# Optimization experiments

Hardware: AMD Instinct MI355X
Metric: run time of the kernel (lower is better)

## Reference

```python
import jax, jax.numpy as jnp
import numpy as np

D, B, L, LS, DH, DU, QK, CD = 5, 2048, 50, 50, 128, 128, 64, 64
EPS = 1e-5

def _l2norm(x):
    n = jnp.linalg.norm(x, axis=-1, keepdims=True)
    return x / jnp.maximum(n, 1e-12)

def setup_inputs() -> dict:
    key = jax.random.key(0)
    ks = jax.random.split(key, 20)
    def pw(k, shape):
        return jax.random.normal(k, shape, dtype=jnp.float32) * 0.02
    return {
        "u": jax.random.normal(ks[0], (B, DU), jnp.float32),
        "H_intra": jax.random.normal(ks[1], (D, B, L, DH), jnp.float32),
        "H_share": jax.random.normal(ks[2], (B, LS, DH), jnp.float32),
        "h": jax.random.normal(ks[3], (B, DH), jnp.float32),
        "domain_ids": jax.random.randint(ks[4], (B,), 0, D),
        "Wq": pw(ks[5], (DU + DH, QK)), "bq": jnp.zeros((QK,), jnp.float32),
        "Wki": pw(ks[6], (DH, QK)), "bki": jnp.zeros((QK,), jnp.float32),
        "Wvi": pw(ks[7], (DH, QK)), "bvi": jnp.zeros((QK,), jnp.float32),
        "Wks": pw(ks[8], (DH, QK)), "bks": jnp.zeros((QK,), jnp.float32),
        "Wvs": pw(ks[9], (DH, QK)), "bvs": jnp.zeros((QK,), jnp.float32),
        "Wf": pw(ks[10], (2 * QK, CD)), "bf": jnp.zeros((CD,), jnp.float32),
        "Wgb": pw(ks[11], (CD, 2 * DH)), "bgb": jnp.zeros((2 * DH,), jnp.float32),
    }

def reference(u, H_intra, H_share, h, domain_ids, Wq, bq, Wki, bki, Wvi, bvi,
              Wks, bks, Wvs, bvs, Wf, bf, Wgb, bgb):
    scale = jnp.sqrt(jnp.asarray(QK, jnp.float32))
    # ---- CDIExtractor (domain loop batched over leading D axis) ----
    c = H_intra.mean(axis=2)                                   # [D,B,DH] ctx = mean over L
    u_b = jnp.broadcast_to(u, (D, B, DU))
    Q = jnp.concatenate([u_b, c], axis=-1) @ Wq + bq            # [D,B,QK]
    Ki = H_intra @ Wki + bki                                    # [D,B,L,QK]
    Vi = H_intra @ Wvi + bvi
    Ks = H_share @ Wks + bks                                    # [B,LS,QK]
    Vs = H_share @ Wvs + bvs
    a_i = jax.nn.softmax(jnp.einsum('dbq,dblq->dbl', Q, Ki) / scale, axis=-1)
    h_i = jnp.einsum('dbl,dblq->dbq', a_i, Vi)                  # [D,B,QK]
    a_s = jax.nn.softmax(jnp.einsum('dbq,blq->dbl', Q, Ks) / scale, axis=-1)
    h_s = jnp.einsum('dbl,blq->dbq', a_s, Vs)                   # [D,B,QK]
    z = jnp.concatenate([h_i, h_s], axis=-1) @ Wf + bf          # [D,B,CD]
    # ---- contrastive loss (stacked as [B,D,QK] like torch.stack(dim=1)) ----
    hi = jnp.transpose(h_i, (1, 0, 2))
    hs = jnp.transpose(h_s, (1, 0, 2))
    ni, ns = _l2norm(hi), _l2norm(hs)
    pos_sim = jnp.sum(ni * ns, axis=-1)                         # [B,D]
    all_sim = jnp.einsum('bdq,beq->bde', ni, ni)                # [B,D,D]
    denom = jnp.exp(all_sim).sum(axis=-1)                       # [B,D]
    L_con = -jnp.mean(jnp.log(jnp.exp(pos_sim) / (denom + 1e-8) + 1e-8))
    # ---- CDIRInjector_Norm (domain-masked AdaNorm, segment statistics) ----
    onehot = jax.nn.one_hot(domain_ids, D, dtype=h.dtype)       # [B,D]
    cnt = jnp.maximum(onehot.sum(axis=0), 1.0)                  # [D]
    mean_d = (onehot.T @ h) / cnt[:, None]                      # [D,DH]
    var_d = (onehot.T @ (h * h)) / cnt[:, None] - mean_d ** 2   # biased var
    mu = mean_d[domain_ids]                                     # [B,DH]
    va = var_d[domain_ids]
    h_norm = (h - mu) / jnp.sqrt(va + EPS)
    z_sel = z[domain_ids, jnp.arange(B)]                        # [B,CD]
    gb = z_sel @ Wgb + bgb
    gamma, beta = jnp.split(gb, 2, axis=-1)
    out = gamma * h_norm + beta + h                             # [B,DH]
    return out, L_con
```

## Files before the change

### kernel.cpp

```cpp
#include <hip/hip_runtime.h>
#include <math.h>

#define D 5
#define B 2048
#define L 50
#define LS 50
#define DH 128
#define DU 128
#define QK 64
#define CD 64
#define EPS 1e-5f

__device__ __forceinline__ float wsum(float v) {
    v += __shfl_xor(v, 1, 64);
    v += __shfl_xor(v, 2, 64);
    v += __shfl_xor(v, 4, 64);
    v += __shfl_xor(v, 8, 64);
    v += __shfl_xor(v, 16, 64);
    v += __shfl_xor(v, 32, 64);
    return v;
}

__device__ __forceinline__ float wmax(float v) {
    v = fmaxf(v, __shfl_xor(v, 1, 64));
    v = fmaxf(v, __shfl_xor(v, 2, 64));
    v = fmaxf(v, __shfl_xor(v, 4, 64));
    v = fmaxf(v, __shfl_xor(v, 8, 64));
    v = fmaxf(v, __shfl_xor(v, 16, 64));
    v = fmaxf(v, __shfl_xor(v, 32, 64));
    return v;
}

__device__ __forceinline__ float gsum32(float v) {
    v += __shfl_xor(v, 1, 64);
    v += __shfl_xor(v, 2, 64);
    v += __shfl_xor(v, 4, 64);
    v += __shfl_xor(v, 8, 64);
    v += __shfl_xor(v, 16, 64);
    return v;
}

__device__ __forceinline__ float dot4(float4 a, float4 b) {
    return a.x * b.x + a.y * b.y + a.z * b.z + a.w * b.w;
}

__global__ __launch_bounds__(256, 6) void kin(
    const float* __restrict__ u,
    const float* __restrict__ Hi,
    const float* __restrict__ Wq, const float* __restrict__ bq,
    const float* __restrict__ Wki,
    const float* __restrict__ Wvi, const float* __restrict__ bvi,
    const float* __restrict__ Wks,
    float* __restrict__ qvs_w,
    float* __restrict__ hi_w)
{
    __shared__ float4 sP4[256];
    __shared__ float sC[DH];
    __shared__ float sPart[4 * QK];
    __shared__ float sQ[QK];
    __shared__ float sQVi[DH];
    __shared__ float sSc[64];
    __shared__ float sA[64];
    __shared__ float sVagg[DH];

    const int b = blockIdx.x, d = blockIdx.y;
    const int t = threadIdx.x;
    const int lane = t & 63;
    const int wave = t >> 6;
    const int g = t >> 5;
    const int col4 = t & 31;
    const int nrow = (g < 2) ? 7 : 6;
    const float* sPf = (const float*)sP4;

    const float* Hbase = Hi + ((size_t)d * B + b) * (L * DH);
    float4 h4[7];
    #pragma unroll
    for (int k = 0; k < 7; ++k) {
        if (k < nrow) h4[k] = *(const float4*)(Hbase + (g + 8 * k) * DH + 4 * col4);
    }

    {
        float4 cs = make_float4(0.f, 0.f, 0.f, 0.f);
        #pragma unroll
        for (int k = 0; k < 7; ++k) {
            if (k < nrow) { cs.x += h4[k].x; cs.y += h4[k].y; cs.z += h4[k].z; cs.w += h4[k].w; }
        }
        sP4[t] = cs;
    }
    __syncthreads();
    if (t < DH) {
        float s = 0.f;
        #pragma unroll
        for (int gg = 0; gg < 8; ++gg) s += sPf[gg * 128 + t];
        sC[t] = s * (1.0f / (float)L);
    }
    __syncthreads();

    {
        float acc = 0.f;
        const int k0 = wave * 48;
        #pragma unroll 8
        for (int i = 0; i < 48; ++i) {
            int k = k0 + i;
            float x = (k < DU) ? u[(size_t)b * DU + k] : sC[k - DU];
            acc += x * Wq[k * QK + lane];
        }
        sPart[wave * QK + lane] = acc;
    }
    __syncthreads();
    if (t < QK) sQ[t] = bq[t] + sPart[t] + sPart[QK + t] + sPart[2 * QK + t] + sPart[3 * QK + t];
    __syncthreads();

    {
        const int colh = t & 127;
        const float* Wkx = (t < 128) ? Wki : Wks;
        const float4* Wr = (const float4*)(Wkx + colh * QK);
        const float4* Qr = (const float4*)sQ;
        float acc = 0.f;
        #pragma unroll
        for (int j = 0; j < 16; ++j) acc += dot4(Wr[j], Qr[j]);
        if (t < 128) sQVi[colh] = acc;
        else qvs_w[((size_t)d * B + b) * DH + colh] = acc;
    }
    __syncthreads();

    {
        float4 qv = ((const float4*)sQVi)[col4];
        #pragma unroll
        for (int k = 0; k < 7; ++k) {
            if (k < nrow) {
                float p = dot4(h4[k], qv);
                p = gsum32(p);
                if (col4 == 0) sSc[g + 8 * k] = p * 0.125f;
            }
        }
    }
    __syncthreads();
    if (wave == 0) {
        float s = (lane < L) ? sSc[lane] : -3.0e38f;
        float m = wmax(s);
        float e = (lane < L) ? expf(s - m) : 0.f;
        float ssum = wsum(e);
        if (lane < L) sA[lane] = e / ssum;
    }
    __syncthreads();

    {
        float4 va = make_float4(0.f, 0.f, 0.f, 0.f);
        #pragma unroll
        for (int k = 0; k < 7; ++k) {
            if (k < nrow) {
                float a = sA[g + 8 * k];
                va.x += a * h4[k].x; va.y += a * h4[k].y;
                va.z += a * h4[k].z; va.w += a * h4[k].w;
            }
        }
        sP4[t] = va;
    }
    __syncthreads();
    if (t < DH) {
        float s = 0.f;
        #pragma unroll
        for (int gg = 0; gg < 8; ++gg) s += sPf[gg * 128 + t];
        sVagg[t] = s;
    }
    __syncthreads();

    {
        float acc = 0.f;
        const int k0 = wave * 32;
        #pragma unroll 8
        for (int i = 0; i < 32; ++i) {
            int k = k0 + i;
            acc += sVagg[k] * Wvi[k * QK + lane];
        }
        sPart[wave * QK + lane] = acc;
    }
    __syncthreads();
    if (t < QK) {
        hi_w[((size_t)d * B + b) * QK + t] =
            bvi[t] + sPart[t] + sPart[QK + t] + sPart[2 * QK + t] + sPart[3 * QK + t];
    }
}

__global__ __launch_bounds__(256) void kstat(
    const float* __restrict__ h, const int* __restrict__ dom_ids,
    float* __restrict__ gsum, float* __restrict__ gsq, float* __restrict__ gcnt)
{
    __shared__ float sS[D * DH], sQ2[D * DH], sCnt[D];
    const int t = threadIdx.x;
    const int b0 = blockIdx.x * 32;
    for (int i = t; i < D * DH; i += 256) { sS[i] = 0.f; sQ2[i] = 0.f; }
    if (t < D) sCnt[t] = 0.f;
    __syncthreads();
    const int col = t & 127, half = t >> 7;
    for (int rr = 0; rr < 16; ++rr) {
        int b = b0 + rr * 2 + half;
        float v = h[(size_t)b * DH + col];
        int dm = dom_ids[b];
        atomicAdd(&sS[dm * DH + col], v);
        atomicAdd(&sQ2[dm * DH + col], v * v);
        if (col == 0) atomicAdd(&sCnt[dm], 1.f);
    }
    __syncthreads();
    for (int i = t; i < D * DH; i += 256) {
        atomicAdd(&gsum[i], sS[i]);
        atomicAdd(&gsq[i], sQ2[i]);
    }
    if (t < D) atomicAdd(&gcnt[t], sCnt[t]);
}

__global__ __launch_bounds__(256, 4) void kfin(
    const float* __restrict__ h, const int* __restrict__ dom_ids,
    const float* __restrict__ Hs,
    const float* __restrict__ qvs_w,
    const float* __restrict__ hi_w,
    const float* __restrict__ Wvs, const float* __restrict__ bvs,
    const float* __restrict__ Wf, const float* __restrict__ bf,
    const float* __restrict__ Wgb, const float* __restrict__ bgb,
    const float* __restrict__ gsum, const float* __restrict__ gsq,
    const float* __restrict__ gcnt,
    float* __restrict__ out, float* __restrict__ loss_out)
{
    __shared__ float4 sQV4[160];
    __shared__ float sHI[D * QK];
    __shared__ float sHS[D * QK];
    __shared__ float sS[D * 64];
    __shared__ float4 sVP4[1280];
    __shared__ float sVA[D * DH];
    __shared__ float sInv[16];
    __shared__ float sSim[32];
    __shared__ float sZ[QK];
    __shared__ float sPartZ[256];
    __shared__ float sGB[256];

    const int b = blockIdx.x;
    const int t = threadIdx.x;
    const int lane = t & 63;
    const int wave = t >> 6;
    const int g = t >> 5;
    const int col4 = t & 31;
    const int nrow = (g < 2) ? 7 : 6;
    float* sBigF = (float*)sVP4;

    const int dm = dom_ids[b];

    const float* Hbase = Hs + (size_t)b * LS * DH;
    float4 h4[7];
    #pragma unroll
    for (int k = 0; k < 7; ++k) {
        if (k < nrow) h4[k] = *(const float4*)(Hbase + (g + 8 * k) * DH + 4 * col4);
    }
    if (t < 160) {
        int dd = t >> 5, c4 = t & 31;
        sQV4[t] = *(const float4*)(qvs_w + ((size_t)dd * B + b) * DH + 4 * c4);
    }
    if (t < 80) {
        int dd = t >> 4, q4 = t & 15;
        ((float4*)sHI)[t] = *(const float4*)(hi_w + ((size_t)dd * B + b) * QK + 4 * q4);
    }
    __syncthreads();

    #pragma unroll
    for (int dd = 0; dd < D; ++dd) {
        float4 qv = sQV4[dd * 32 + col4];
        #pragma unroll
        for (int k = 0; k < 7; ++k) {
            if (k < nrow) {
                float p = dot4(h4[k], qv);
                p = gsum32(p);
                if (col4 == 0) sS[dd * 64 + g + 8 * k] = p * 0.125f;
            }
        }
    }
    __syncthreads();
    for (int dd = wave; dd < D; dd += 4) {
        float s = (lane < LS) ? sS[dd * 64 + lane] : -3.0e38f;
        float m = wmax(s);
        float e = (lane < LS) ? expf(s - m) : 0.f;
        float ssum = wsum(e);
        if (lane < LS) sS[dd * 64 + lane] = e / ssum;
    }
    __syncthreads();

    {
        float4 va[D];
        #pragma unroll
        for (int dd = 0; dd < D; ++dd) va[dd] = make_float4(0.f, 0.f, 0.f, 0.f);
        #pragma unroll
        for (int k = 0; k < 7; ++k) {
            if (k < nrow) {
                float4 hv = h4[k];
                #pragma unroll
                for (int dd = 0; dd < D; ++dd) {
                    float a = sS[dd * 64 + g + 8 * k];
                    va[dd].x += a * hv.x; va[dd].y += a * hv.y;
                    va[dd].z += a * hv.z; va[dd].w += a * hv.w;
                }
            }
        }
        #pragma unroll
        for (int dd = 0; dd < D; ++dd) sVP4[dd * 256 + t] = va[dd];
    }
    __syncthreads();
    for (int o = t; o < D * DH; o += 256) {
        int dd = o >> 7, col = o & 127;
        float s = 0.f;
        #pragma unroll
        for (int gg = 0; gg < 8; ++gg) s += sBigF[dd * 1024 + gg * 128 + col];
        sVA[o] = s;
    }
    __syncthreads();

    #pragma unroll
    for (int j = 0; j < 5; ++j) {
        int tau = t + j * 256;
        int kq = tau / 320;
        int o = tau - kq * 320;
        int dd = o >> 6, q = o & 63;
        float acc = 0.f;
        const int k0 = kq * 32;
        #pragma unroll 8
        for (int i = 0; i < 32; ++i) {
            int k = k0 + i;
            acc += sVA[dd * 128 + k] * Wvs[k * QK + q];
        }
        sBigF[tau] = acc;
    }
    __syncthreads();
    for (int o = t; o < D * QK; o += 256) {
        int q = o & 63;
        sHS[o] = bvs[q] + sBigF[o] + sBigF[o + 320] + sBigF[o + 640] + sBigF[o + 960];
    }
    __syncthreads();

    for (int v = wave; v < 2 * D; v += 4) {
        float x = (v < D) ? sHI[v * QK + lane] : sHS[(v - D) * QK + lane];
        float ss = wsum(x * x);
        if (lane == 0) sInv[v] = 1.0f / fmaxf(sqrtf(ss), 1e-12f);
    }
    __syncthreads();
    for (int p = wave; p < 30; p += 4) {
        float s;
        if (p < 25) {
            int dd = p / 5, e = p - dd * 5;
            s = wsum(sHI[dd * QK + lane] * sHI[e * QK + lane] * sInv[dd] * sInv[e]);
        } else {
            int dd = p - 25;
            s = wsum(sHI[dd * QK + lane] * sHS[dd * QK + lane] * sInv[dd] * sInv[D + dd]);
        }
        if (lane == 0) sSim[p] = s;
    }
    __syncthreads();
    if (t == 0) {
        float tot = 0.f;
        #pragma unroll
        for (int dd = 0; dd < D; ++dd) {
            float den = 0.f;
            #pragma unroll
            for (int e = 0; e < D; ++e) den += expf(sSim[dd * 5 + e]);
            tot += logf(expf(sSim[25 + dd]) / (den + 1e-8f) + 1e-8f);
        }
        atomicAdd(loss_out, -tot / (float)(B * D));
    }

    {
        const int kq = wave, q = lane;
        float acc = 0.f;
        const int k0 = kq * 32;
        #pragma unroll 8
        for (int i = 0; i < 32; ++i) {
            int k = k0 + i;
            float x = (k < QK) ? sHI[dm * QK + k] : sHS[dm * QK + (k - QK)];
            acc += x * Wf[k * CD + q];
        }
        sPartZ[t] = acc;
    }
    __syncthreads();
    if (t < QK) sZ[t] = bf[t] + sPartZ[t] + sPartZ[64 + t] + sPartZ[128 + t] + sPartZ[192 + t];
    __syncthreads();

    {
        float acc = bgb[t];
        #pragma unroll 8
        for (int k = 0; k < CD; ++k) acc += sZ[k] * Wgb[k * (2 * DH) + t];
        sGB[t] = acc;
    }
    __syncthreads();

    if (t < DH) {
        float c = fmaxf(gcnt[dm], 1.0f);
        float mu = gsum[dm * DH + t] / c;
        float va = gsq[dm * DH + t] / c - mu * mu;
        float hv = h[(size_t)b * DH + t];
        float hn = (hv - mu) / sqrtf(va + EPS);
        out[(size_t)b * DH + t] = sGB[t] * hn + sGB[DH + t] + hv;
    }
}

extern "C" void kernel_launch(void* const* d_in, const int* in_sizes, int n_in,
                              void* d_out, int out_size, void* d_ws, size_t ws_size,
                              hipStream_t stream)
{
    (void)in_sizes; (void)n_in; (void)out_size; (void)ws_size;
    const float* u   = (const float*)d_in[0];
    const float* Hi  = (const float*)d_in[1];
    const float* Hs  = (const float*)d_in[2];
    const float* h   = (const float*)d_in[3];
    const int*   dom = (const int*)d_in[4];
    const float* Wq  = (const float*)d_in[5];
    const float* bq  = (const float*)d_in[6];
    const float* Wki = (const float*)d_in[7];
    const float* Wvi = (const float*)d_in[9];
    const float* bvi = (const float*)d_in[10];
    const float* Wks = (const float*)d_in[11];
    const float* Wvs = (const float*)d_in[13];
    const float* bvs = (const float*)d_in[14];
    const float* Wf  = (const float*)d_in[15];
    const float* bf  = (const float*)d_in[16];
    const float* Wgb = (const float*)d_in[17];
    const float* bgb = (const float*)d_in[18];

    float* out = (float*)d_out;
    float* loss_out = out + (size_t)B * DH;

    float* ws = (float*)d_ws;
    float* qvs_w = ws;
    float* hi_w  = qvs_w + (size_t)D * B * DH;
    float* gsum  = hi_w + (size_t)D * B * QK;
    float* gsq   = gsum + D * DH;
    float* gcnt  = gsq + D * DH;

    hipMemsetAsync(gsum, 0, (size_t)(2 * D * DH + 8) * sizeof(float), stream);
    hipMemsetAsync(loss_out, 0, sizeof(float), stream);

    hipLaunchKernelGGL(kstat, dim3(B / 32), dim3(256), 0, stream, h, dom, gsum, gsq, gcnt);
    hipLaunchKernelGGL(kin, dim3(B, D), dim3(256), 0, stream,
                       u, Hi, Wq, bq, Wki, Wvi, bvi, Wks, qvs_w, hi_w);
    hipLaunchKernelGGL(kfin, dim3(B), dim3(256), 0, stream,
                       h, dom, Hs, qvs_w, hi_w, Wvs, bvs, Wf, bf, Wgb, bgb,
                       gsum, gsq, gcnt, out, loss_out);
}
```

Measured before the change: 612.7 us.

## Precompute Wq·Wk products and u-projections, process two batch rows per block

The query-key projection is refactored algebraically. Wq_c·Wk^T (Gi/Gs) and the u part of the query times Wk are precomputed in a new setup kernel, so each (d,b) block only does a 128x128 matvec on the context mean instead of recomputing Q and Q·Wk. The kin kernel now handles two batch rows per block so each G and Wvi load is reused twice. kfin is split into a shared-attention kernel and a final kernel, which adds a workspace round-trip for h_s and two extra launches. Register pressure rises, since each thread holds 13 float4 values and the launch bound drops from 6 to 4 blocks.

```diff
diff --git a/kernel.cpp b/kernel.cpp
--- a/kernel.cpp
+++ b/kernel.cpp
@@ -44,142 +44,186 @@
     return a.x * b.x + a.y * b.y + a.z * b.z + a.w * b.w;
 }
 
-__global__ __launch_bounds__(256, 6) void kin(
+__global__ __launch_bounds__(256) void ksetup(
     const float* __restrict__ u,
+    const float* __restrict__ Wq, const float* __restrict__ bq,
+    const float* __restrict__ Wki, const float* __restrict__ Wks,
+    float* __restrict__ Gi, float* __restrict__ Gs,
+    float* __restrict__ qu_i, float* __restrict__ qu_s)
+{
+    const int t = threadIdx.x;
+    if (blockIdx.x < DH) {
+        __shared__ float sWqc[QK];
+        const int j = blockIdx.x;
+        if (t < QK) sWqc[t] = Wq[(DU + j) * QK + t];
+        __syncthreads();
+        const int k = t & 127;
+        const float* Wk = (t < 128) ? Wki : Wks;
+        const float4* Wr = (const float4*)(Wk + k * QK);
+        const float4* cq = (const float4*)sWqc;
+        float acc = 0.f;
+        #pragma unroll
+        for (int q4 = 0; q4 < 16; ++q4) acc += dot4(Wr[q4], cq[q4]);
+        if (t < 128) Gi[j * DH + k] = acc;
+        else Gs[j * DH + k] = acc;
+    } else {
+        __shared__ float sPart[4 * QK];
+        __shared__ float sQu[QK];
+        const int b = blockIdx.x - DH;
+        const int lane = t & 63, wave = t >> 6;
+        float acc = 0.f;
+        const int k0 = wave * 32;
+        #pragma unroll 8
+        for (int i = 0; i < 32; ++i) {
+            int k = k0 + i;
+            acc += u[(size_t)b * DU + k] * Wq[k * QK + lane];
+        }
+        sPart[wave * QK + lane] = acc;
+        __syncthreads();
+        if (t < QK) sQu[t] = bq[t] + sPart[t] + sPart[64 + t] + sPart[128 + t] + sPart[192 + t];
+        __syncthreads();
+        const int k = t & 127;
+        const float* Wk = (t < 128) ? Wki : Wks;
+        const float4* Wr = (const float4*)(Wk + k * QK);
+        const float4* cq = (const float4*)sQu;
+        float acc2 = 0.f;
+        #pragma unroll
+        for (int q4 = 0; q4 < 16; ++q4) acc2 += dot4(Wr[q4], cq[q4]);
+        if (t < 128) qu_i[(size_t)b * DH + k] = acc2;
+        else qu_s[(size_t)b * DH + k] = acc2;
+    }
+}
+
+__global__ __launch_bounds__(256, 4) void kin(
     const float* __restrict__ Hi,
-    const float* __restrict__ Wq, const float* __restrict__ bq,
-    const float* __restrict__ Wki,
+    const float* __restrict__ Gi, const float* __restrict__ Gs,
+    const float* __restrict__ qu_i, const float* __restrict__ qu_s,
     const float* __restrict__ Wvi, const float* __restrict__ bvi,
-    const float* __restrict__ Wks,
     float* __restrict__ qvs_w,
     float* __restrict__ hi_w)
 {
     __shared__ float4 sP4[256];
-    __shared__ float sC[DH];
-    __shared__ float sPart[4 * QK];
-    __shared__ float sQ[QK];
-    __shared__ float sQVi[DH];
-    __shared__ float sSc[64];
-    __shared__ float sA[64];
-    __shared__ float sVagg[DH];
-
-    const int b = blockIdx.x, d = blockIdx.y;
+    __shared__ float sC2[2 * DH];
+    __shared__ float sQVi[2 * DH];
+    __shared__ float sSc[128];
+    __shared__ float sA[128];
+    __shared__ float sVagg[2 * DH];
+    __shared__ float sPA[256], sPB[256];
+
+    const int b0 = blockIdx.x * 2;
+    const int d = blockIdx.y;
     const int t = threadIdx.x;
-    const int lane = t & 63;
-    const int wave = t >> 6;
-    const int g = t >> 5;
+    const int lane = t & 63, wave = t >> 6;
+    const int bb = t >> 7;
+    const int tb = t & 127;
+    const int gg = tb >> 5;
     const int col4 = t & 31;
-    const int nrow = (g < 2) ? 7 : 6;
+    const int nr = (gg < 2) ? 13 : 12;
     const float* sPf = (const float*)sP4;
 
-    const float* Hbase = Hi + ((size_t)d * B + b) * (L * DH);
-    float4 h4[7];
+    const float* Hbase = Hi + ((size_t)d * B + (b0 + bb)) * (L * DH);
+    float4 h4[13];
     #pragma unroll
-    for (int k = 0; k < 7; ++k) {
-        if (k < nrow) h4[k] = *(const float4*)(Hbase + (g + 8 * k) * DH + 4 * col4);
-    }
+    for (int k = 0; k < 13; ++k)
+        if (k < nr) h4[k] = *(const float4*)(Hbase + (gg + 4 * k) * DH + 4 * col4);
 
     {
         float4 cs = make_float4(0.f, 0.f, 0.f, 0.f);
         #pragma unroll
-        for (int k = 0; k < 7; ++k) {
-            if (k < nrow) { cs.x += h4[k].x; cs.y += h4[k].y; cs.z += h4[k].z; cs.w += h4[k].w; }
-        }
+        for (int k = 0; k < 13; ++k)
+            if (k < nr) { cs.x += h4[k].x; cs.y += h4[k].y; cs.z += h4[k].z; cs.w += h4[k].w; }
         sP4[t] = cs;
     }
     __syncthreads();
-    if (t < DH) {
-        float s = 0.f;
-        #pragma unroll
-        for (int gg = 0; gg < 8; ++gg) s += sPf[gg * 128 + t];
-        sC[t] = s * (1.0f / (float)L);
-    }
-    __syncthreads();
-
-    {
-        float acc = 0.f;
-        const int k0 = wave * 48;
-        #pragma unroll 8
-        for (int i = 0; i < 48; ++i) {
-            int k = k0 + i;
-            float x = (k < DU) ? u[(size_t)b * DU + k] : sC[k - DU];
-            acc += x * Wq[k * QK + lane];
-        }
-        sPart[wave * QK + lane] = acc;
-    }
-    __syncthreads();
-    if (t < QK) sQ[t] = bq[t] + sPart[t] + sPart[QK + t] + sPart[2 * QK + t] + sPart[3 * QK + t];
-    __syncthreads();
-
-    {
-        const int colh = t & 127;
-        const float* Wkx = (t < 128) ? Wki : Wks;
-        const float4* Wr = (const float4*)(Wkx + colh * QK);
-        const float4* Qr = (const float4*)sQ;
-        float acc = 0.f;
-        #pragma unroll
-        for (int j = 0; j < 16; ++j) acc += dot4(Wr[j], Qr[j]);
-        if (t < 128) sQVi[colh] = acc;
-        else qvs_w[((size_t)d * B + b) * DH + colh] = acc;
-    }
-    __syncthreads();
-
-    {
-        float4 qv = ((const float4*)sQVi)[col4];
-        #pragma unroll
-        for (int k = 0; k < 7; ++k) {
-            if (k < nrow) {
+    {
+        const int bbc = t >> 7, col = t & 127;
+        float s = sPf[bbc * 512 + col] + sPf[bbc * 512 + 128 + col]
+                + sPf[bbc * 512 + 256 + col] + sPf[bbc * 512 + 384 + col];
+        sC2[col * 2 + bbc] = s * (1.0f / (float)L);
+    }
+    __syncthreads();
+
+    {
+        const int mat = t >> 7, k = t & 127;
+        const float* G = mat ? Gs : Gi;
+        const float* qum = mat ? qu_s : qu_i;
+        float a0 = qum[(size_t)b0 * DH + k];
+        float a1 = qum[(size_t)(b0 + 1) * DH + k];
+        const float2* c2 = (const float2*)sC2;
+        #pragma unroll 8
+        for (int j = 0; j < DH; ++j) {
+            float g = G[j * DH + k];
+            float2 c = c2[j];
+            a0 += c.x * g;
+            a1 += c.y * g;
+        }
+        if (mat == 0) { sQVi[k] = a0; sQVi[DH + k] = a1; }
+        else {
+            qvs_w[((size_t)d * B + b0) * DH + k] = a0;
+            qvs_w[((size_t)d * B + b0 + 1) * DH + k] = a1;
+        }
+    }
+    __syncthreads();
+
+    {
+        float4 qv = ((const float4*)sQVi)[bb * 32 + col4];
+        #pragma unroll
+        for (int k = 0; k < 13; ++k)
+            if (k < nr) {
                 float p = dot4(h4[k], qv);
                 p = gsum32(p);
-                if (col4 == 0) sSc[g + 8 * k] = p * 0.125f;
+                if (col4 == 0) sSc[bb * 64 + gg + 4 * k] = p * 0.125f;
             }
-        }
-    }
-    __syncthreads();
-    if (wave == 0) {
-        float s = (lane < L) ? sSc[lane] : -3.0e38f;
+    }
+    __syncthreads();
+    if (wave < 2) {
+        float s = (lane < L) ? sSc[wave * 64 + lane] : -3.0e38f;
         float m = wmax(s);
         float e = (lane < L) ? expf(s - m) : 0.f;
         float ssum = wsum(e);
-        if (lane < L) sA[lane] = e / ssum;
+        if (lane < L) sA[wave * 64 + lane] = e / ssum;
     }
     __syncthreads();
 
     {
         float4 va = make_float4(0.f, 0.f, 0.f, 0.f);
         #pragma unroll
-        for (int k = 0; k < 7; ++k) {
-            if (k < nrow) {
-                float a = sA[g + 8 * k];
+        for (int k = 0; k < 13; ++k)
+            if (k < nr) {
+                float a = sA[bb * 64 + gg + 4 * k];
                 va.x += a * h4[k].x; va.y += a * h4[k].y;
                 va.z += a * h4[k].z; va.w += a * h4[k].w;
             }
-        }
         sP4[t] = va;
     }
     __syncthreads();
-    if (t < DH) {
-        float s = 0.f;
-        #pragma unroll
-        for (int gg = 0; gg < 8; ++gg) s += sPf[gg * 128 + t];
-        sVagg[t] = s;
-    }
-    __syncthreads();
-
-    {
-        float acc = 0.f;
-        const int k0 = wave * 32;
+    {
+        const int bbc = t >> 7, col = t & 127;
+        sVagg[bbc * 128 + col] = sPf[bbc * 512 + col] + sPf[bbc * 512 + 128 + col]
+                               + sPf[bbc * 512 + 256 + col] + sPf[bbc * 512 + 384 + col];
+    }
+    __syncthreads();
+
+    {
+        const int q = t & 63, kq = t >> 6;
+        const int k0 = kq * 32;
+        float a0 = 0.f, a1 = 0.f;
         #pragma unroll 8
         for (int i = 0; i < 32; ++i) {
             int k = k0 + i;
-            acc += sVagg[k] * Wvi[k * QK + lane];
-        }
-        sPart[wave * QK + lane] = acc;
-    }
-    __syncthreads();
-    if (t < QK) {
-        hi_w[((size_t)d * B + b) * QK + t] =
-            bvi[t] + sPart[t] + sPart[QK + t] + sPart[2 * QK + t] + sPart[3 * QK + t];
+            float w = Wvi[k * QK + q];
+            a0 += sVagg[k] * w;
+            a1 += sVagg[128 + k] * w;
+        }
+        sPA[kq * 64 + q] = a0;
+        sPB[kq * 64 + q] = a1;
+    }
+    __syncthreads();
+    if (t < 128) {
+        const int bw = t >> 6, q = t & 63;
+        const float* P = bw ? sPB : sPA;
+        hi_w[((size_t)d * B + b0 + bw) * QK + q] =
+            bvi[q] + P[q] + P[64 + q] + P[128 + q] + P[192 + q];
     }
 }
 
@@ -210,29 +254,16 @@
     if (t < D) atomicAdd(&gcnt[t], sCnt[t]);
 }
 
-__global__ __launch_bounds__(256, 4) void kfin(
-    const float* __restrict__ h, const int* __restrict__ dom_ids,
+__global__ __launch_bounds__(256, 4) void ksh(
     const float* __restrict__ Hs,
     const float* __restrict__ qvs_w,
-    const float* __restrict__ hi_w,
     const float* __restrict__ Wvs, const float* __restrict__ bvs,
-    const float* __restrict__ Wf, const float* __restrict__ bf,
-    const float* __restrict__ Wgb, const float* __restrict__ bgb,
-    const float* __restrict__ gsum, const float* __restrict__ gsq,
-    const float* __restrict__ gcnt,
-    float* __restrict__ out, float* __restrict__ loss_out)
+    float* __restrict__ hs_w)
 {
     __shared__ float4 sQV4[160];
-    __shared__ float sHI[D * QK];
-    __shared__ float sHS[D * QK];
     __shared__ float sS[D * 64];
     __shared__ float4 sVP4[1280];
     __shared__ float sVA[D * DH];
-    __shared__ float sInv[16];
-    __shared__ float sSim[32];
-    __shared__ float sZ[QK];
-    __shared__ float sPartZ[256];
-    __shared__ float sGB[256];
 
     const int b = blockIdx.x;
     const int t = threadIdx.x;
@@ -243,35 +274,27 @@
     const int nrow = (g < 2) ? 7 : 6;
     float* sBigF = (float*)sVP4;
 
-    const int dm = dom_ids[b];
-
     const float* Hbase = Hs + (size_t)b * LS * DH;
     float4 h4[7];
     #pragma unroll
-    for (int k = 0; k < 7; ++k) {
+    for (int k = 0; k < 7; ++k)
         if (k < nrow) h4[k] = *(const float4*)(Hbase + (g + 8 * k) * DH + 4 * col4);
-    }
     if (t < 160) {
         int dd = t >> 5, c4 = t & 31;
         sQV4[t] = *(const float4*)(qvs_w + ((size_t)dd * B + b) * DH + 4 * c4);
     }
-    if (t < 80) {
-        int dd = t >> 4, q4 = t & 15;
-        ((float4*)sHI)[t] = *(const float4*)(hi_w + ((size_t)dd * B + b) * QK + 4 * q4);
-    }
     __syncthreads();
 
     #pragma unroll
     for (int dd = 0; dd < D; ++dd) {
         float4 qv = sQV4[dd * 32 + col4];
         #pragma unroll
-        for (int k = 0; k < 7; ++k) {
+        for (int k = 0; k < 7; ++k)
             if (k < nrow) {
                 float p = dot4(h4[k], qv);
                 p = gsum32(p);
                 if (col4 == 0) sS[dd * 64 + g + 8 * k] = p * 0.125f;
             }
-        }
     }
     __syncthreads();
     for (int dd = wave; dd < D; dd += 4) {
@@ -288,7 +311,7 @@
         #pragma unroll
         for (int dd = 0; dd < D; ++dd) va[dd] = make_float4(0.f, 0.f, 0.f, 0.f);
         #pragma unroll
-        for (int k = 0; k < 7; ++k) {
+        for (int k = 0; k < 7; ++k)
             if (k < nrow) {
                 float4 hv = h4[k];
                 #pragma unroll
@@ -298,7 +321,6 @@
                     va[dd].z += a * hv.z; va[dd].w += a * hv.w;
                 }
             }
-        }
         #pragma unroll
         for (int dd = 0; dd < D; ++dd) sVP4[dd * 256 + t] = va[dd];
     }
@@ -329,8 +351,34 @@
     }
     __syncthreads();
     for (int o = t; o < D * QK; o += 256) {
-        int q = o & 63;
-        sHS[o] = bvs[q] + sBigF[o] + sBigF[o + 320] + sBigF[o + 640] + sBigF[o + 960];
+        int dd = o >> 6, q = o & 63;
+        hs_w[((size_t)dd * B + b) * QK + q] =
+            bvs[q] + sBigF[o] + sBigF[o + 320] + sBigF[o + 640] + sBigF[o + 960];
+    }
+}
+
+__global__ __launch_bounds__(256) void kfin(
+    const float* __restrict__ h, const int* __restrict__ dom_ids,
+    const float* __restrict__ hi_w, const float* __restrict__ hs_w,
+    const float* __restrict__ Wf, const float* __restrict__ bf,
+    const float* __restrict__ Wgb, const float* __restrict__ bgb,
+    const float* __restrict__ gsum, const float* __restrict__ gsq,
+    const float* __restrict__ gcnt,
+    float* __restrict__ out, float* __restrict__ loss_out)
+{
+    __shared__ float sHI[D * QK], sHS[D * QK];
+    __shared__ float sInv[16], sSim[32], sZ[QK], sPartZ[256], sGB[256];
+
+    const int b = blockIdx.x;
+    const int t = threadIdx.x;
+    const int lane = t & 63;
+    const int wave = t >> 6;
+    const int dm = dom_ids[b];
+
+    if (t < 80) {
+        int dd = t >> 4, q4 = t & 15;
+        ((float4*)sHI)[t] = *(const float4*)(hi_w + ((size_t)dd * B + b) * QK + 4 * q4);
+        ((float4*)sHS)[t] = *(const float4*)(hs_w + ((size_t)dd * B + b) * QK + 4 * q4);
     }
     __syncthreads();
 
@@ -425,19 +473,26 @@
     float* loss_out = out + (size_t)B * DH;
 
     float* ws = (float*)d_ws;
-    float* qvs_w = ws;
+    float* Gi    = ws;
+    float* Gs    = Gi + DH * DH;
+    float* qu_i  = Gs + DH * DH;
+    float* qu_s  = qu_i + (size_t)B * DH;
+    float* qvs_w = qu_s + (size_t)B * DH;
     float* hi_w  = qvs_w + (size_t)D * B * DH;
-    float* gsum  = hi_w + (size_t)D * B * QK;
+    float* hs_w  = hi_w + (size_t)D * B * QK;
+    float* gsum  = hs_w + (size_t)D * B * QK;
     float* gsq   = gsum + D * DH;
     float* gcnt  = gsq + D * DH;
 
     hipMemsetAsync(gsum, 0, (size_t)(2 * D * DH + 8) * sizeof(float), stream);
     hipMemsetAsync(loss_out, 0, sizeof(float), stream);
 
+    hipLaunchKernelGGL(ksetup, dim3(DH + B), dim3(256), 0, stream,
+                       u, Wq, bq, Wki, Wks, Gi, Gs, qu_i, qu_s);
     hipLaunchKernelGGL(kstat, dim3(B / 32), dim3(256), 0, stream, h, dom, gsum, gsq, gcnt);
-    hipLaunchKernelGGL(kin, dim3(B, D), dim3(256), 0, stream,
-                       u, Hi, Wq, bq, Wki, Wvi, bvi, Wks, qvs_w, hi_w);
+    hipLaunchKernelGGL(kin, dim3(B / 2, D), dim3(256), 0, stream,
+                       Hi, Gi, Gs, qu_i, qu_s, Wvi, bvi, qvs_w, hi_w);
+    hipLaunchKernelGGL(ksh, dim3(B), dim3(256), 0, stream, Hs, qvs_w, Wvs, bvs, hs_w);
     hipLaunchKernelGGL(kfin, dim3(B), dim3(256), 0, stream,
-                       h, dom, Hs, qvs_w, hi_w, Wvs, bvs, Wf, bf, Wgb, bgb,
-                       gsum, gsq, gcnt, out, loss_out);
-}
+                       h, dom, hi_w, hs_w, Wf, bf, Wgb, bgb, gsum, gsq, gcnt, out, loss_out);
+}
```

Result: faster. 560.1 us (-8.6%).
